# Optimization experiments

Hardware: AMD Instinct MI355X
Metric: run time of the kernel (lower is better)

The kernel has to match this reference:

```python
import jax, jax.numpy as jnp
import numpy as np

N_NODES = 349525  # complete 4-ary tree, depth 10: (4**10 - 1) / 3
X_SIZE = 128
H_SIZE = 128


def setup_inputs() -> dict:
    key = jax.random.key(0)
    ks = jax.random.split(key, 6)
    s = 0.05  # keep gates out of saturation
    return {
        "x": jax.random.normal(ks[0], (N_NODES, X_SIZE), jnp.float32),
        "W_iou": jax.random.normal(ks[1], (X_SIZE, 3 * H_SIZE), jnp.float32) * s,
        "U_iou": jax.random.normal(ks[2], (H_SIZE, 3 * H_SIZE), jnp.float32) * s,
        "b_iou": jnp.zeros((3 * H_SIZE,), jnp.float32),
        "W_f": jax.random.normal(ks[3], (X_SIZE, H_SIZE), jnp.float32) * s,
        "U_f": jax.random.normal(ks[4], (H_SIZE, H_SIZE), jnp.float32) * s,
        "b_f": jnp.zeros((H_SIZE,), jnp.float32),
        "depth": 10,
        "branching": 4,
    }


def _apply_node(iou, c_sum):
    # apply_node_func: i,o,u gates then cell/hidden update
    i, o, u = jnp.split(iou, 3, axis=-1)
    c = jax.nn.sigmoid(i) * jnp.tanh(u) + c_sum
    h = jax.nn.sigmoid(o) * jnp.tanh(c)
    return h, c


def reference(x, W_iou, U_iou, b_iou, W_f, U_f, b_f, depth, branching):
    # Nodes are in BFS order of a complete `branching`-ary forest-tree;
    # level l occupies [off[l], off[l+1]) and the children of level l are
    # exactly level l+1 (contiguous, `branching` per parent).
    H = b_f.shape[-1]
    off = [(branching ** l - 1) // (branching - 1) for l in range(depth + 1)]

    node_iou = x @ W_iou + b_iou  # [N, 3H]  (W_iou(x) + b_iou)
    node_f = x @ W_f + b_f        # [N, H]   (W_f(x) + b_f)

    h_levels = [None] * depth
    c_levels = [None] * depth

    # Leaves: mailbox empty -> h_tilda = 0, c = 0
    s, e = off[depth - 1], off[depth]
    h, c = _apply_node(node_iou[s:e], jnp.zeros((e - s, H), x.dtype))
    h_levels[depth - 1], c_levels[depth - 1] = h, c

    # Bottom-up topological propagation
    for l in range(depth - 2, -1, -1):
        s, e = off[l], off[l + 1]
        nl = e - s
        ch_h = h_levels[l + 1].reshape(nl, branching, H)  # mailbox['h']
        ch_c = c_levels[l + 1].reshape(nl, branching, H)  # mailbox['c']
        h_tilda = ch_h.sum(axis=1)
        # f = sigmoid(U_f(mailbox.h) + node_f[:, None])
        f = jax.nn.sigmoid(jnp.einsum("nkh,hg->nkg", ch_h, U_f) + node_f[s:e][:, None, :])
        c_sum = (f * ch_c).sum(axis=1)
        iou = node_iou[s:e] + h_tilda @ U_iou
        h, c = _apply_node(iou, c_sum)
        h_levels[l], c_levels[l] = h, c

    h_all = jnp.concatenate(h_levels, axis=0)
    c_all = jnp.concatenate(c_levels, axis=0)
    return h_all, c_all
```

## Files before the change

### kernel.cpp

```cpp
#include <hip/hip_runtime.h>

#define H 128

typedef __bf16 bf16x8 __attribute__((ext_vector_type(8)));
typedef float f32x4 __attribute__((ext_vector_type(4)));

__device__ __forceinline__ float fsig(float x) {
  return __builtin_amdgcn_rcpf(1.0f + __expf(-x));
}
__device__ __forceinline__ float ftanh(float x) {
  float ax = fabsf(x), e = __expf(-2.0f * ax);
  float t = (1.0f - e) * __builtin_amdgcn_rcpf(1.0f + e);
  return x < 0.0f ? -t : t;
}
__device__ __forceinline__ uint2 pack4(float a, float b, float c, float d) {
  union { __bf16 h[4]; uint2 u; } r;
  r.h[0] = (__bf16)a; r.h[1] = (__bf16)b; r.h[2] = (__bf16)c; r.h[3] = (__bf16)d;
  return r.u;
}
__device__ __forceinline__ unsigned short bfbits(float h) {
  union { __bf16 b; unsigned short u; } cv; cv.b = (__bf16)h; return cv.u;
}
__device__ __forceinline__ unsigned swz(unsigned row, unsigned colByte, unsigned rowBytes) {
  return (row * rowBytes + colByte) ^ ((row & 7) << 4);
}

__global__ __launch_bounds__(256)
void prep_weights(const float* __restrict__ W_iou, const float* __restrict__ U_iou,
                  const float* __restrict__ W_f, const float* __restrict__ U_f,
                  uint4* __restrict__ ws)
{
  int item = blockIdx.x * 256 + threadIdx.x;
  float v[8];
  if (item < 2048) {
    int fj = item >> 8, rem = item & 255, ks = rem >> 6, lane = rem & 63;
    int n = fj * 16 + (lane & 15), kb = ks * 32 + (lane >> 4) * 8;
    #pragma unroll
    for (int j = 0; j < 8; j++) v[j] = U_f[(kb + j) * H + n];
  } else if (item < 4096) {
    int i2 = item - 2048;
    int fj = i2 >> 8, rem = i2 & 255, ks = rem >> 6, lane = rem & 63;
    int n = fj * 16 + (lane & 15), kb = ks * 32 + (lane >> 4) * 8;
    #pragma unroll
    for (int j = 0; j < 8; j++) v[j] = W_f[(kb + j) * H + n];
  } else {
    int i2 = item - 4096;
    int fj = i2 >> 9, rem = i2 & 511, ks = rem >> 6, lane = rem & 63;
    int col = (fj >> 3) * 128 + (fj & 7) * 16 + (lane & 15);
    int kb = ks * 32 + (lane >> 4) * 8;
    #pragma unroll
    for (int j = 0; j < 8; j++) {
      int k = kb + j;
      v[j] = (k < 128) ? W_iou[k * 384 + col] : U_iou[(k - 128) * 384 + col];
    }
  }
  union { __bf16 h[8]; uint4 u; } r;
  #pragma unroll
  for (int j = 0; j < 8; j++) r.h[j] = (__bf16)v[j];
  ws[item] = r.u;
}

__device__ __forceinline__ void leaf_half(const char* As, const __bf16* __restrict__ iou_fmt,
                                          int j, int w, int l15, int l4, int lane,
                                          f32x4 (&acc)[4][3])
{
  #pragma unroll
  for (int ks = 0; ks < 4; ks++) {
    bf16x8 a[4], b[3];
    #pragma unroll
    for (int m = 0; m < 4; m++)
      a[m] = *reinterpret_cast<const bf16x8*>(As + swz(m * 16 + l15, (ks * 32 + l4 * 8) * 2, 256));
    #pragma unroll
    for (int g = 0; g < 3; g++) {
      int nf = g * 8 + 2 * w + j;
      b[g] = *reinterpret_cast<const bf16x8*>(iou_fmt + ((size_t)(nf * 8 + ks) * 64 + lane) * 8);
    }
    #pragma unroll
    for (int m = 0; m < 4; m++)
      #pragma unroll
      for (int g = 0; g < 3; g++)
        acc[m][g] = __builtin_amdgcn_mfma_f32_16x16x32_bf16(a[m], b[g], acc[m][g], 0, 0, 0);
  }
}

template<bool WS>
__global__ __launch_bounds__(256)
void leaf8(const float* __restrict__ x, const __bf16* __restrict__ iou_fmt,
           const float* __restrict__ b_iou,
           float* __restrict__ h_glob, float* __restrict__ c_glob,
           __bf16* __restrict__ hb_dst, int leaf_start)
{
  __shared__ __align__(16) char As[64 * 256];
  const int t = threadIdx.x;
  const int bid = blockIdx.x;
  const int m0 = leaf_start + bid * 64;
  const int lane = t & 63, w = t >> 6;
  const int l15 = lane & 15, l4 = lane >> 4;

  #pragma unroll
  for (int i = 0; i < 8; i++) {
    int idx = t + i * 256;
    int r = idx >> 5, k0 = (idx & 31) << 2;
    f32x4 v = *reinterpret_cast<const f32x4*>(&x[(size_t)(m0 + r) * H + k0]);
    *reinterpret_cast<uint2*>(As + swz(r, k0 * 2, 256)) = pack4(v.x, v.y, v.z, v.w);
  }
  __syncthreads();

  unsigned hj0p[8];

  {
    f32x4 acc[4][3] = {};
    leaf_half(As, iou_fmt, 0, w, l15, l4, lane, acc);
    int ch = 2 * w * 16 + l15;
    float bi = b_iou[ch], bo = b_iou[H + ch], bu = b_iou[2 * H + ch];
    #pragma unroll
    for (int m = 0; m < 4; m++) {
      int rowb = m * 16 + l4 * 4;
      unsigned hv[4];
      #pragma unroll
      for (int r = 0; r < 4; r++) {
        size_t o = (size_t)(m0 + rowb + r) * H + ch;
        float c = fsig(acc[m][0][r] + bi) * ftanh(acc[m][2][r] + bu);
        float h = fsig(acc[m][1][r] + bo) * ftanh(c);
        h_glob[o] = h;
        c_glob[o] = c;
        if (WS) hv[r] = bfbits(h);
      }
      if (WS) {
        hj0p[m * 2 + 0] = hv[0] | (hv[1] << 16);
        hj0p[m * 2 + 1] = hv[2] | (hv[3] << 16);
      }
    }
  }

  {
    f32x4 acc[4][3] = {};
    leaf_half(As, iou_fmt, 1, w, l15, l4, lane, acc);
    __syncthreads();
    int ch = (2 * w + 1) * 16 + l15;
    float bi = b_iou[ch], bo = b_iou[H + ch], bu = b_iou[2 * H + ch];
    #pragma unroll
    for (int m = 0; m < 4; m++) {
      int rowb = m * 16 + l4 * 4;
      #pragma unroll
      for (int r = 0; r < 4; r++) {
        size_t o = (size_t)(m0 + rowb + r) * H + ch;
        float c = fsig(acc[m][0][r] + bi) * ftanh(acc[m][2][r] + bu);
        float h = fsig(acc[m][1][r] + bo) * ftanh(c);
        h_glob[o] = h;
        c_glob[o] = c;
        if (WS)
          *reinterpret_cast<unsigned short*>(As + swz(rowb + r, ch * 2, 256)) = bfbits(h);
      }
    }
  }

  if (WS) {
    int ch0 = 2 * w * 16 + l15;
    #pragma unroll
    for (int m = 0; m < 4; m++) {
      int rowb = m * 16 + l4 * 4;
      #pragma unroll
      for (int r = 0; r < 4; r++) {
        unsigned hv = hj0p[m * 2 + (r >> 1)] >> ((r & 1) * 16);
        *reinterpret_cast<unsigned short*>(As + swz(rowb + r, ch0 * 2, 256)) = (unsigned short)hv;
      }
    }
    __syncthreads();
    char* dst = reinterpret_cast<char*>(hb_dst) + (size_t)bid * 64 * 256;
    #pragma unroll
    for (int i = 0; i < 4; i++) {
      int idx = t + i * 256;
      int row = idx >> 4, chunk = idx & 15;
      uint4 v = *reinterpret_cast<const uint4*>(As + swz(row, chunk * 16, 256));
      *reinterpret_cast<uint4*>(dst + row * 256 + chunk * 16) = v;
    }
  }
}

template<bool HB>
__device__ __forceinline__ void fused_core(
    const __bf16* __restrict__ uf_fmt, const __bf16* __restrict__ wf_fmt,
    const __bf16* __restrict__ iou_fmt,
    const float* __restrict__ b_iou, const float* __restrict__ b_f,
    float* __restrict__ h_glob, float* __restrict__ c_glob,
    int prow0, int crow0, int npar,
    char* CH, char* XH, float* SC)
{
  const int t = threadIdx.x;
  const int lane = t & 63, w = t >> 6;
  const int l15 = lane & 15, l4 = lane >> 4;

  {
    f32x4 acc[2][2] = {};
    #pragma unroll
    for (int ks = 0; ks < 4; ks++) {
      bf16x8 a[2], b[2];
      #pragma unroll
      for (int m = 0; m < 2; m++)
        a[m] = *reinterpret_cast<const bf16x8*>(XH + swz(m * 16 + l15, (ks * 32 + l4 * 8) * 2, 512));
      #pragma unroll
      for (int n = 0; n < 2; n++) {
        int nf = 2 * w + n;
        b[n] = *reinterpret_cast<const bf16x8*>(wf_fmt + ((size_t)(nf * 4 + ks) * 64 + lane) * 8);
      }
      #pragma unroll
      for (int m = 0; m < 2; m++)
        #pragma unroll
        for (int n = 0; n < 2; n++)
          acc[m][n] = __builtin_amdgcn_mfma_f32_16x16x32_bf16(a[m], b[n], acc[m][n], 0, 0, 0);
    }
    #pragma unroll
    for (int m = 0; m < 2; m++)
      #pragma unroll
      for (int n = 0; n < 2; n++)
        #pragma unroll
        for (int r = 0; r < 4; r++)
          SC[(m * 16 + l4 * 4 + r) * 128 + (2 * w + n) * 16 + l15] = acc[m][n][r];
  }
  __syncthreads();

  {
    f32x4 acc[2][8] = {};
    #pragma unroll
    for (int ks = 0; ks < 4; ks++) {
      bf16x8 a[2], b[8];
      #pragma unroll
      for (int m = 0; m < 2; m++)
        a[m] = *reinterpret_cast<const bf16x8*>(CH + swz(w * 32 + m * 16 + l15, (ks * 32 + l4 * 8) * 2, 256));
      #pragma unroll
      for (int n = 0; n < 8; n++)
        b[n] = *reinterpret_cast<const bf16x8*>(uf_fmt + ((size_t)(n * 4 + ks) * 64 + lane) * 8);
      #pragma unroll
      for (int m = 0; m < 2; m++)
        #pragma unroll
        for (int n = 0; n < 8; n++)
          acc[m][n] = __builtin_amdgcn_mfma_f32_16x16x32_bf16(a[m], b[n], acc[m][n], 0, 0, 0);
    }
    #pragma unroll
    for (int m = 0; m < 2; m++) {
      int rbase = w * 32 + m * 16 + l4 * 4;
      int ploc = rbase >> 2;
      #pragma unroll
      for (int n = 0; n < 8; n++) {
        int ch = n * 16 + l15;
        float sfx = SC[ploc * 128 + ch] + b_f[ch];
        float cs = 0.0f;
        #pragma unroll
        for (int r = 0; r < 4; r++) {
          float f = fsig(acc[m][n][r] + sfx);
          cs = fmaf(f, c_glob[(size_t)(crow0 + rbase + r) * H + ch], cs);
        }
        SC[ploc * 128 + ch] = cs;
      }
    }
  }
  __syncthreads();

  {
    f32x4 acc[2][3][2] = {};
    #pragma unroll
    for (int ks = 0; ks < 8; ks++) {
      bf16x8 a[2], b[3][2];
      #pragma unroll
      for (int m = 0; m < 2; m++)
        a[m] = *reinterpret_cast<const bf16x8*>(XH + swz(m * 16 + l15, (ks * 32 + l4 * 8) * 2, 512));
      #pragma unroll
      for (int g = 0; g < 3; g++)
        #pragma unroll
        for (int j = 0; j < 2; j++) {
          int nf = g * 8 + 2 * w + j;
          b[g][j] = *reinterpret_cast<const bf16x8*>(iou_fmt + ((size_t)(nf * 8 + ks) * 64 + lane) * 8);
        }
      #pragma unroll
      for (int m = 0; m < 2; m++)
        #pragma unroll
        for (int g = 0; g < 3; g++)
          #pragma unroll
          for (int j = 0; j < 2; j++)
            acc[m][g][j] = __builtin_amdgcn_mfma_f32_16x16x32_bf16(a[m], b[g][j], acc[m][g][j], 0, 0, 0);
    }
    #pragma unroll
    for (int j = 0; j < 2; j++) {
      int ch = (2 * w + j) * 16 + l15;
      float bi = b_iou[ch], bo = b_iou[H + ch], bu = b_iou[2 * H + ch];
      #pragma unroll
      for (int m = 0; m < 2; m++) {
        #pragma unroll
        for (int r = 0; r < 4; r++) {
          int ploc = m * 16 + l4 * 4 + r;
          if (ploc < npar) {
            float gi = acc[m][0][j][r] + bi;
            float go = acc[m][1][j][r] + bo;
            float gu = acc[m][2][j][r] + bu;
            float cs = SC[ploc * 128 + ch];
            float c = fsig(gi) * ftanh(gu) + cs;
            float h = fsig(go) * ftanh(c);
            size_t o = (size_t)(prow0 + ploc) * H + ch;
            h_glob[o] = h;
            c_glob[o] = c;
            if (HB)
              *reinterpret_cast<unsigned short*>(CH + swz(ploc, ch * 2, 256)) = bfbits(h);
          }
        }
      }
    }
  }
}

template<bool WRITE_HB>
__global__ __launch_bounds__(256)
void fused_hb(const float* __restrict__ x, const __bf16* __restrict__ uf_fmt,
              const __bf16* __restrict__ wf_fmt, const __bf16* __restrict__ iou_fmt,
              const float* __restrict__ b_iou, const float* __restrict__ b_f,
              float* __restrict__ h_glob, float* __restrict__ c_glob,
              const __bf16* __restrict__ ch_src, __bf16* __restrict__ hb_dst,
              int pstart, int cstart)
{
  __shared__ __align__(16) char CH[128 * 256];
  __shared__ __align__(16) char XH[32 * 512];
  __shared__ float SC[32 * 128];
  const int t = threadIdx.x;
  const int bid = blockIdx.x;

  {
    const char* csrc = reinterpret_cast<const char*>(ch_src) + (size_t)bid * 128 * 256;
    #pragma unroll
    for (int i = 0; i < 8; i++) {
      int idx = t + i * 256;
      int row = idx >> 4, chunk = idx & 15;
      uint4 v = *reinterpret_cast<const uint4*>(csrc + row * 256 + chunk * 16);
      *reinterpret_cast<uint4*>(CH + swz(row, chunk * 16, 256)) = v;
    }
  }
  #pragma unroll
  for (int i = 0; i < 4; i++) {
    int idx = t + i * 256;
    int p = idx >> 5, k0 = (idx & 31) << 2;
    f32x4 v = *reinterpret_cast<const f32x4*>(&x[(size_t)(pstart + bid * 32 + p) * H + k0]);
    *reinterpret_cast<uint2*>(XH + swz(p, k0 * 2, 512)) = pack4(v.x, v.y, v.z, v.w);
  }
  __syncthreads();
  #pragma unroll
  for (int i = 0; i < 2; i++) {
    int idx = t + i * 256;
    int p = idx >> 4, chunk = idx & 15;
    float s[8] = {};
    #pragma unroll
    for (int cj = 0; cj < 4; cj++) {
      union { uint4 u; __bf16 h[8]; } uv;
      uv.u = *reinterpret_cast<const uint4*>(CH + swz(4 * p + cj, chunk * 16, 256));
      #pragma unroll
      for (int e = 0; e < 8; e++) s[e] += (float)uv.h[e];
    }
    union { __bf16 h[8]; uint4 u; } ov;
    #pragma unroll
    for (int e = 0; e < 8; e++) ov.h[e] = (__bf16)s[e];
    *reinterpret_cast<uint4*>(XH + swz(p, 256 + chunk * 16, 512)) = ov.u;
  }
  __syncthreads();

  fused_core<WRITE_HB>(uf_fmt, wf_fmt, iou_fmt, b_iou, b_f, h_glob, c_glob,
                       pstart + bid * 32, cstart + bid * 128, 32, CH, XH, SC);

  if (WRITE_HB) {
    __syncthreads();
    char* dst = reinterpret_cast<char*>(hb_dst) + (size_t)bid * 32 * 256;
    #pragma unroll
    for (int i = 0; i < 2; i++) {
      int idx = t + i * 256;
      int row = idx >> 4, chunk = idx & 15;
      uint4 v = *reinterpret_cast<const uint4*>(CH + swz(row, chunk * 16, 256));
      *reinterpret_cast<uint4*>(dst + row * 256 + chunk * 16) = v;
    }
  }
}

__device__ __forceinline__ void fused_body(
    const float* __restrict__ x, const __bf16* __restrict__ uf_fmt,
    const __bf16* __restrict__ wf_fmt, const __bf16* __restrict__ iou_fmt,
    const float* __restrict__ b_iou, const float* __restrict__ b_f,
    float* __restrict__ h_glob, float* __restrict__ c_glob,
    int prow0, int crow0, int npar,
    char* CH, char* XH, float* SC)
{
  const int t = threadIdx.x;
  #pragma unroll
  for (int i = 0; i < 4; i++) {
    int idx = t + i * 256;
    int p = idx >> 5, k0 = (idx & 31) << 2;
    f32x4 s = {};
    #pragma unroll
    for (int j = 0; j < 4; j++) {
      f32x4 v = *reinterpret_cast<const f32x4*>(&h_glob[(size_t)(crow0 + p * 4 + j) * H + k0]);
      *reinterpret_cast<uint2*>(CH + swz(p * 4 + j, k0 * 2, 256)) = pack4(v.x, v.y, v.z, v.w);
      s += v;
    }
    *reinterpret_cast<uint2*>(XH + swz(p, (128 + k0) * 2, 512)) = pack4(s.x, s.y, s.z, s.w);
  }
  #pragma unroll
  for (int i = 0; i < 4; i++) {
    int idx = t + i * 256;
    int p = idx >> 5, k0 = (idx & 31) << 2;
    f32x4 v = *reinterpret_cast<const f32x4*>(&x[(size_t)(prow0 + p) * H + k0]);
    *reinterpret_cast<uint2*>(XH + swz(p, k0 * 2, 512)) = pack4(v.x, v.y, v.z, v.w);
  }
  __syncthreads();
  fused_core<false>(uf_fmt, wf_fmt, iou_fmt, b_iou, b_f, h_glob, c_glob,
                    prow0, crow0, npar, CH, XH, SC);
}

__global__ __launch_bounds__(256)
void fused_level(const float* __restrict__ x, const __bf16* __restrict__ uf_fmt,
                 const __bf16* __restrict__ wf_fmt, const __bf16* __restrict__ iou_fmt,
                 const float* __restrict__ b_iou, const float* __restrict__ b_f,
                 float* __restrict__ h_glob, float* __restrict__ c_glob,
                 int pstart, int cstart)
{
  __shared__ __align__(16) char CH[128 * 256];
  __shared__ __align__(16) char XH[32 * 512];
  __shared__ float SC[32 * 128];
  fused_body(x, uf_fmt, wf_fmt, iou_fmt, b_iou, b_f, h_glob, c_glob,
             pstart + blockIdx.x * 32, cstart + blockIdx.x * 128, 32, CH, XH, SC);
}

#define SNR 4
#define SRP 2
#define BR 4

__global__ __launch_bounds__(256)
void small_kernel(const float* __restrict__ x,
                  const float* __restrict__ W_iou, const float* __restrict__ b_iou,
                  const float* __restrict__ U_iou, const float* __restrict__ W_f,
                  const float* __restrict__ U_f, const float* __restrict__ b_f,
                  float* __restrict__ h_out, float* __restrict__ c_out,
                  int lvl_start, int child_start, int n_lvl)
{
  __shared__ float xs[SNR][H];
  __shared__ float hs[SNR * BR][H];
  __shared__ float ht[SNR][H];
  const int t = threadIdx.x;
  const int node0 = blockIdx.x * SNR;
  const int nrows = min(SNR, n_lvl - node0);

  {
    const f32x4* xgv = reinterpret_cast<const f32x4*>(x + (size_t)(lvl_start + node0) * H);
    f32x4* xsv = reinterpret_cast<f32x4*>(&xs[0][0]);
    int total = nrows * (H / 4);
    for (int i = t; i < total; i += 256) xsv[i] = xgv[i];
  }
  {
    const f32x4* hgv = reinterpret_cast<const f32x4*>(h_out + (size_t)(child_start + node0 * BR) * H);
    f32x4* hsv = reinterpret_cast<f32x4*>(&hs[0][0]);
    int total = nrows * BR * (H / 4);
    for (int i = t; i < total; i += 256) hsv[i] = hgv[i];
  }
  __syncthreads();

  const int ch = t & (H - 1);
  const int g = t >> 7;

  float fx[SRP], ai[SRP], ao[SRP], au[SRP];
  {
    float bi = b_iou[ch], bo = b_iou[ch + H], bu = b_iou[ch + 2 * H], bf = b_f[ch];
    #pragma unroll
    for (int r = 0; r < SRP; r++) { fx[r] = bf; ai[r] = bi; ao[r] = bo; au[r] = bu; }
  }
  {
    const float* wfp = W_f + ch;
    const float* wip = W_iou + ch;
    #pragma unroll 4
    for (int k = 0; k < H; k++) {
      float wf = wfp[k * H];
      float w0 = wip[k * 384], w1 = wip[k * 384 + H], w2 = wip[k * 384 + 2 * H];
      #pragma unroll
      for (int r = 0; r < SRP; r++) {
        float xk = xs[g * SRP + r][k];
        fx[r] = fmaf(xk, wf, fx[r]);
        ai[r] = fmaf(xk, w0, ai[r]);
        ao[r] = fmaf(xk, w1, ao[r]);
        au[r] = fmaf(xk, w2, au[r]);
      }
    }
  }
  #pragma unroll
  for (int r = 0; r < SRP; r++) {
    int row = g * SRP + r;
    float s = hs[row * BR + 0][ch] + hs[row * BR + 1][ch]
            + hs[row * BR + 2][ch] + hs[row * BR + 3][ch];
    ht[row][ch] = s;
  }
  __syncthreads();

  float z[BR][SRP];
  #pragma unroll
  for (int kc = 0; kc < BR; kc++)
    #pragma unroll
    for (int r = 0; r < SRP; r++) z[kc][r] = fx[r];
  {
    const float* ufp = U_f + ch;
    #pragma unroll 4
    for (int m = 0; m < H; m++) {
      float uf = ufp[m * H];
      #pragma unroll
      for (int kc = 0; kc < BR; kc++)
        #pragma unroll
        for (int r = 0; r < SRP; r++)
          z[kc][r] = fmaf(hs[(g * SRP + r) * BR + kc][m], uf, z[kc][r]);
    }
  }
  float csum[SRP];
  #pragma unroll
  for (int r = 0; r < SRP; r++) csum[r] = 0.0f;
  #pragma unroll
  for (int kc = 0; kc < BR; kc++) {
    #pragma unroll
    for (int r = 0; r < SRP; r++) {
      size_t childnode = (size_t)child_start + (size_t)(node0 + g * SRP + r) * BR + kc;
      float f = fsig(z[kc][r]);
      csum[r] = fmaf(f, c_out[childnode * H + ch], csum[r]);
    }
  }
  {
    const float* uip = U_iou + ch;
    #pragma unroll 4
    for (int m = 0; m < H; m++) {
      float w0 = uip[m * 384], w1 = uip[m * 384 + H], w2 = uip[m * 384 + 2 * H];
      #pragma unroll
      for (int r = 0; r < SRP; r++) {
        float hm = ht[g * SRP + r][m];
        ai[r] = fmaf(hm, w0, ai[r]);
        ao[r] = fmaf(hm, w1, ao[r]);
        au[r] = fmaf(hm, w2, au[r]);
      }
    }
  }
  #pragma unroll
  for (int r = 0; r < SRP; r++) {
    int row = g * SRP + r;
    if (row < nrows) {
      float c = fsig(ai[r]) * ftanh(au[r]) + csum[r];
      float h = fsig(ao[r]) * ftanh(c);
      size_t node = (size_t)(lvl_start + node0 + row);
      h_out[node * H + ch] = h;
      c_out[node * H + ch] = c;
    }
  }
}

extern "C" void kernel_launch(void* const* d_in, const int* in_sizes, int n_in,
                              void* d_out, int out_size, void* d_ws, size_t ws_size,
                              hipStream_t stream)
{
  const float* x     = (const float*)d_in[0];
  const float* W_iou = (const float*)d_in[1];
  const float* U_iou = (const float*)d_in[2];
  const float* b_iou = (const float*)d_in[3];
  const float* W_f   = (const float*)d_in[4];
  const float* U_f   = (const float*)d_in[5];
  const float* b_f   = (const float*)d_in[6];
  const int N = 349525;

  float* h_out = (float*)d_out;
  float* c_out = h_out + (size_t)N * H;

  const __bf16* uf_fmt  = (const __bf16*)d_ws;
  const __bf16* wf_fmt  = (const __bf16*)d_ws + 16384;
  const __bf16* iou_fmt = (const __bf16*)d_ws + 32768;
  __bf16* hb16 = (__bf16*)((char*)d_ws + 262144);
  __bf16* hb_l8 = hb16 + (size_t)262144 * 128;

  const bool use_ws = ws_size >= (262144ULL + 83886080ULL);

  int off[11];
  off[0] = 0;
  for (int l = 1; l <= 10; l++) off[l] = off[l - 1] * 4 + 1;

  prep_weights<<<64, 256, 0, stream>>>(W_iou, U_iou, W_f, U_f, (uint4*)d_ws);

  if (use_ws) {
    leaf8<true><<<4096, 256, 0, stream>>>(x, iou_fmt, b_iou, h_out, c_out, hb16, off[9]);
    fused_hb<true><<<2048, 256, 0, stream>>>(x, uf_fmt, wf_fmt, iou_fmt, b_iou, b_f,
                                             h_out, c_out, hb16, hb_l8, off[8], off[9]);
    fused_hb<false><<<512, 256, 0, stream>>>(x, uf_fmt, wf_fmt, iou_fmt, b_iou, b_f,
                                             h_out, c_out, hb_l8, nullptr, off[7], off[8]);
  } else {
    leaf8<false><<<4096, 256, 0, stream>>>(x, iou_fmt, b_iou, h_out, c_out, nullptr, off[9]);
    fused_level<<<2048, 256, 0, stream>>>(x, uf_fmt, wf_fmt, iou_fmt, b_iou, b_f,
                                          h_out, c_out, off[8], off[9]);
    fused_level<<<512, 256, 0, stream>>>(x, uf_fmt, wf_fmt, iou_fmt, b_iou, b_f,
                                         h_out, c_out, off[7], off[8]);
  }

  for (int l = 6; l >= 4; l--) {
    int n_par = off[l + 1] - off[l];
    fused_level<<<n_par / 32, 256, 0, stream>>>(x, uf_fmt, wf_fmt, iou_fmt, b_iou, b_f,
                                                h_out, c_out, off[l], off[l + 1]);
  }

  for (int l = 3; l >= 0; l--) {
    int s = off[l], e = off[l + 1];
    int n = e - s;
    int grid = (n + SNR - 1) / SNR;
    small_kernel<<<grid, 256, 0, stream>>>(x, W_iou, b_iou, U_iou, W_f, U_f, b_f,
                                           h_out, c_out, s, e, n);
  }
}
```

Before: 384.9 us.

## Split fused level kernels across 512 threads with one MFMA column tile per wave

Fused internal-level kernels now launch 512 threads (8 waves) instead of 256, and each wave handles half the previous MFMA tiles. The W_f and iou GEMMs give each wave one 16-column tile instead of two, and the U_f child GEMM gives each wave 16 child rows instead of 32. Load and store loops are rescaled to match. This aims to raise wave-level parallelism and cut per-thread register pressure for latency hiding, at the cost of more waves per block and more redundant A-fragment loads from LDS.

```diff
diff --git a/kernel.cpp b/kernel.cpp
--- a/kernel.cpp
+++ b/kernel.cpp
@@ -179,7 +179,7 @@
 }
 
 template<bool HB>
-__device__ __forceinline__ void fused_core(
+__device__ __forceinline__ void fused_core512(
     const __bf16* __restrict__ uf_fmt, const __bf16* __restrict__ wf_fmt,
     const __bf16* __restrict__ iou_fmt,
     const float* __restrict__ b_iou, const float* __restrict__ b_f,
@@ -192,116 +192,94 @@
   const int l15 = lane & 15, l4 = lane >> 4;
 
   {
-    f32x4 acc[2][2] = {};
+    f32x4 acc[2] = {};
     #pragma unroll
     for (int ks = 0; ks < 4; ks++) {
-      bf16x8 a[2], b[2];
+      bf16x8 a[2], b;
       #pragma unroll
       for (int m = 0; m < 2; m++)
         a[m] = *reinterpret_cast<const bf16x8*>(XH + swz(m * 16 + l15, (ks * 32 + l4 * 8) * 2, 512));
-      #pragma unroll
-      for (int n = 0; n < 2; n++) {
-        int nf = 2 * w + n;
-        b[n] = *reinterpret_cast<const bf16x8*>(wf_fmt + ((size_t)(nf * 4 + ks) * 64 + lane) * 8);
-      }
+      b = *reinterpret_cast<const bf16x8*>(wf_fmt + ((size_t)(w * 4 + ks) * 64 + lane) * 8);
       #pragma unroll
       for (int m = 0; m < 2; m++)
-        #pragma unroll
-        for (int n = 0; n < 2; n++)
-          acc[m][n] = __builtin_amdgcn_mfma_f32_16x16x32_bf16(a[m], b[n], acc[m][n], 0, 0, 0);
+        acc[m] = __builtin_amdgcn_mfma_f32_16x16x32_bf16(a[m], b, acc[m], 0, 0, 0);
     }
     #pragma unroll
     for (int m = 0; m < 2; m++)
       #pragma unroll
-      for (int n = 0; n < 2; n++)
-        #pragma unroll
-        for (int r = 0; r < 4; r++)
-          SC[(m * 16 + l4 * 4 + r) * 128 + (2 * w + n) * 16 + l15] = acc[m][n][r];
-  }
-  __syncthreads();
-
-  {
-    f32x4 acc[2][8] = {};
+      for (int r = 0; r < 4; r++)
+        SC[(m * 16 + l4 * 4 + r) * 128 + w * 16 + l15] = acc[m][r];
+  }
+  __syncthreads();
+
+  {
+    f32x4 acc[8] = {};
     #pragma unroll
     for (int ks = 0; ks < 4; ks++) {
-      bf16x8 a[2], b[8];
-      #pragma unroll
-      for (int m = 0; m < 2; m++)
-        a[m] = *reinterpret_cast<const bf16x8*>(CH + swz(w * 32 + m * 16 + l15, (ks * 32 + l4 * 8) * 2, 256));
+      bf16x8 a, b[8];
+      a = *reinterpret_cast<const bf16x8*>(CH + swz(w * 16 + l15, (ks * 32 + l4 * 8) * 2, 256));
       #pragma unroll
       for (int n = 0; n < 8; n++)
         b[n] = *reinterpret_cast<const bf16x8*>(uf_fmt + ((size_t)(n * 4 + ks) * 64 + lane) * 8);
       #pragma unroll
-      for (int m = 0; m < 2; m++)
-        #pragma unroll
-        for (int n = 0; n < 8; n++)
-          acc[m][n] = __builtin_amdgcn_mfma_f32_16x16x32_bf16(a[m], b[n], acc[m][n], 0, 0, 0);
-    }
-    #pragma unroll
-    for (int m = 0; m < 2; m++) {
-      int rbase = w * 32 + m * 16 + l4 * 4;
-      int ploc = rbase >> 2;
-      #pragma unroll
-      for (int n = 0; n < 8; n++) {
-        int ch = n * 16 + l15;
-        float sfx = SC[ploc * 128 + ch] + b_f[ch];
-        float cs = 0.0f;
-        #pragma unroll
-        for (int r = 0; r < 4; r++) {
-          float f = fsig(acc[m][n][r] + sfx);
-          cs = fmaf(f, c_glob[(size_t)(crow0 + rbase + r) * H + ch], cs);
-        }
-        SC[ploc * 128 + ch] = cs;
-      }
-    }
-  }
-  __syncthreads();
-
-  {
-    f32x4 acc[2][3][2] = {};
+      for (int n = 0; n < 8; n++)
+        acc[n] = __builtin_amdgcn_mfma_f32_16x16x32_bf16(a, b[n], acc[n], 0, 0, 0);
+    }
+    int rbase = w * 16 + l4 * 4;
+    int ploc = rbase >> 2;
+    #pragma unroll
+    for (int n = 0; n < 8; n++) {
+      int ch = n * 16 + l15;
+      float sfx = SC[ploc * 128 + ch] + b_f[ch];
+      float cs = 0.0f;
+      #pragma unroll
+      for (int r = 0; r < 4; r++) {
+        float f = fsig(acc[n][r] + sfx);
+        cs = fmaf(f, c_glob[(size_t)(crow0 + rbase + r) * H + ch], cs);
+      }
+      SC[ploc * 128 + ch] = cs;
+    }
+  }
+  __syncthreads();
+
+  {
+    f32x4 acc[2][3] = {};
     #pragma unroll
     for (int ks = 0; ks < 8; ks++) {
-      bf16x8 a[2], b[3][2];
+      bf16x8 a[2], b[3];
       #pragma unroll
       for (int m = 0; m < 2; m++)
         a[m] = *reinterpret_cast<const bf16x8*>(XH + swz(m * 16 + l15, (ks * 32 + l4 * 8) * 2, 512));
       #pragma unroll
-      for (int g = 0; g < 3; g++)
-        #pragma unroll
-        for (int j = 0; j < 2; j++) {
-          int nf = g * 8 + 2 * w + j;
-          b[g][j] = *reinterpret_cast<const bf16x8*>(iou_fmt + ((size_t)(nf * 8 + ks) * 64 + lane) * 8);
-        }
+      for (int g = 0; g < 3; g++) {
+        int nf = g * 8 + w;
+        b[g] = *reinterpret_cast<const bf16x8*>(iou_fmt + ((size_t)(nf * 8 + ks) * 64 + lane) * 8);
+      }
       #pragma unroll
       for (int m = 0; m < 2; m++)
         #pragma unroll
         for (int g = 0; g < 3; g++)
-          #pragma unroll
-          for (int j = 0; j < 2; j++)
-            acc[m][g][j] = __builtin_amdgcn_mfma_f32_16x16x32_bf16(a[m], b[g][j], acc[m][g][j], 0, 0, 0);
-    }
-    #pragma unroll
-    for (int j = 0; j < 2; j++) {
-      int ch = (2 * w + j) * 16 + l15;
-      float bi = b_iou[ch], bo = b_iou[H + ch], bu = b_iou[2 * H + ch];
-      #pragma unroll
-      for (int m = 0; m < 2; m++) {
-        #pragma unroll
-        for (int r = 0; r < 4; r++) {
-          int ploc = m * 16 + l4 * 4 + r;
-          if (ploc < npar) {
-            float gi = acc[m][0][j][r] + bi;
-            float go = acc[m][1][j][r] + bo;
-            float gu = acc[m][2][j][r] + bu;
-            float cs = SC[ploc * 128 + ch];
-            float c = fsig(gi) * ftanh(gu) + cs;
-            float h = fsig(go) * ftanh(c);
-            size_t o = (size_t)(prow0 + ploc) * H + ch;
-            h_glob[o] = h;
-            c_glob[o] = c;
-            if (HB)
-              *reinterpret_cast<unsigned short*>(CH + swz(ploc, ch * 2, 256)) = bfbits(h);
-          }
+          acc[m][g] = __builtin_amdgcn_mfma_f32_16x16x32_bf16(a[m], b[g], acc[m][g], 0, 0, 0);
+    }
+    int ch = w * 16 + l15;
+    float bi = b_iou[ch], bo = b_iou[H + ch], bu = b_iou[2 * H + ch];
+    #pragma unroll
+    for (int m = 0; m < 2; m++) {
+      #pragma unroll
+      for (int r = 0; r < 4; r++) {
+        int ploc = m * 16 + l4 * 4 + r;
+        if (ploc < npar) {
+          float gi = acc[m][0][r] + bi;
+          float go = acc[m][1][r] + bo;
+          float gu = acc[m][2][r] + bu;
+          float cs = SC[ploc * 128 + ch];
+          float c = fsig(gi) * ftanh(gu) + cs;
+          float h = fsig(go) * ftanh(c);
+          size_t o = (size_t)(prow0 + ploc) * H + ch;
+          h_glob[o] = h;
+          c_glob[o] = c;
+          if (HB)
+            *reinterpret_cast<unsigned short*>(CH + swz(ploc, ch * 2, 256)) = bfbits(h);
         }
       }
     }
@@ -309,7 +287,7 @@
 }
 
 template<bool WRITE_HB>
-__global__ __launch_bounds__(256)
+__global__ __launch_bounds__(512)
 void fused_hb(const float* __restrict__ x, const __bf16* __restrict__ uf_fmt,
               const __bf16* __restrict__ wf_fmt, const __bf16* __restrict__ iou_fmt,
               const float* __restrict__ b_iou, const float* __restrict__ b_f,
@@ -326,25 +304,23 @@
   {
     const char* csrc = reinterpret_cast<const char*>(ch_src) + (size_t)bid * 128 * 256;
     #pragma unroll
-    for (int i = 0; i < 8; i++) {
-      int idx = t + i * 256;
+    for (int i = 0; i < 4; i++) {
+      int idx = t + i * 512;
       int row = idx >> 4, chunk = idx & 15;
       uint4 v = *reinterpret_cast<const uint4*>(csrc + row * 256 + chunk * 16);
       *reinterpret_cast<uint4*>(CH + swz(row, chunk * 16, 256)) = v;
     }
   }
   #pragma unroll
-  for (int i = 0; i < 4; i++) {
-    int idx = t + i * 256;
+  for (int i = 0; i < 2; i++) {
+    int idx = t + i * 512;
     int p = idx >> 5, k0 = (idx & 31) << 2;
     f32x4 v = *reinterpret_cast<const f32x4*>(&x[(size_t)(pstart + bid * 32 + p) * H + k0]);
     *reinterpret_cast<uint2*>(XH + swz(p, k0 * 2, 512)) = pack4(v.x, v.y, v.z, v.w);
   }
   __syncthreads();
-  #pragma unroll
-  for (int i = 0; i < 2; i++) {
-    int idx = t + i * 256;
-    int p = idx >> 4, chunk = idx & 15;
+  {
+    int p = t >> 4, chunk = t & 15;
     float s[8] = {};
     #pragma unroll
     for (int cj = 0; cj < 4; cj++) {
@@ -360,57 +336,19 @@
   }
   __syncthreads();
 
-  fused_core<WRITE_HB>(uf_fmt, wf_fmt, iou_fmt, b_iou, b_f, h_glob, c_glob,
-                       pstart + bid * 32, cstart + bid * 128, 32, CH, XH, SC);
+  fused_core512<WRITE_HB>(uf_fmt, wf_fmt, iou_fmt, b_iou, b_f, h_glob, c_glob,
+                          pstart + bid * 32, cstart + bid * 128, 32, CH, XH, SC);
 
   if (WRITE_HB) {
     __syncthreads();
     char* dst = reinterpret_cast<char*>(hb_dst) + (size_t)bid * 32 * 256;
-    #pragma unroll
-    for (int i = 0; i < 2; i++) {
-      int idx = t + i * 256;
-      int row = idx >> 4, chunk = idx & 15;
-      uint4 v = *reinterpret_cast<const uint4*>(CH + swz(row, chunk * 16, 256));
-      *reinterpret_cast<uint4*>(dst + row * 256 + chunk * 16) = v;
-    }
-  }
-}
-
-__device__ __forceinline__ void fused_body(
-    const float* __restrict__ x, const __bf16* __restrict__ uf_fmt,
-    const __bf16* __restrict__ wf_fmt, const __bf16* __restrict__ iou_fmt,
-    const float* __restrict__ b_iou, const float* __restrict__ b_f,
-    float* __restrict__ h_glob, float* __restrict__ c_glob,
-    int prow0, int crow0, int npar,
-    char* CH, char* XH, float* SC)
-{
-  const int t = threadIdx.x;
-  #pragma unroll
-  for (int i = 0; i < 4; i++) {
-    int idx = t + i * 256;
-    int p = idx >> 5, k0 = (idx & 31) << 2;
-    f32x4 s = {};
-    #pragma unroll
-    for (int j = 0; j < 4; j++) {
-      f32x4 v = *reinterpret_cast<const f32x4*>(&h_glob[(size_t)(crow0 + p * 4 + j) * H + k0]);
-      *reinterpret_cast<uint2*>(CH + swz(p * 4 + j, k0 * 2, 256)) = pack4(v.x, v.y, v.z, v.w);
-      s += v;
-    }
-    *reinterpret_cast<uint2*>(XH + swz(p, (128 + k0) * 2, 512)) = pack4(s.x, s.y, s.z, s.w);
-  }
-  #pragma unroll
-  for (int i = 0; i < 4; i++) {
-    int idx = t + i * 256;
-    int p = idx >> 5, k0 = (idx & 31) << 2;
-    f32x4 v = *reinterpret_cast<const f32x4*>(&x[(size_t)(prow0 + p) * H + k0]);
-    *reinterpret_cast<uint2*>(XH + swz(p, k0 * 2, 512)) = pack4(v.x, v.y, v.z, v.w);
-  }
-  __syncthreads();
-  fused_core<false>(uf_fmt, wf_fmt, iou_fmt, b_iou, b_f, h_glob, c_glob,
-                    prow0, crow0, npar, CH, XH, SC);
-}
-
-__global__ __launch_bounds__(256)
+    int row = t >> 4, chunk = t & 15;
+    uint4 v = *reinterpret_cast<const uint4*>(CH + swz(row, chunk * 16, 256));
+    *reinterpret_cast<uint4*>(dst + row * 256 + chunk * 16) = v;
+  }
+}
+
+__global__ __launch_bounds__(512)
 void fused_level(const float* __restrict__ x, const __bf16* __restrict__ uf_fmt,
                  const __bf16* __restrict__ wf_fmt, const __bf16* __restrict__ iou_fmt,
                  const float* __restrict__ b_iou, const float* __restrict__ b_f,
@@ -420,8 +358,33 @@
   __shared__ __align__(16) char CH[128 * 256];
   __shared__ __align__(16) char XH[32 * 512];
   __shared__ float SC[32 * 128];
-  fused_body(x, uf_fmt, wf_fmt, iou_fmt, b_iou, b_f, h_glob, c_glob,
-             pstart + blockIdx.x * 32, cstart + blockIdx.x * 128, 32, CH, XH, SC);
+  const int t = threadIdx.x;
+  const int prow0 = pstart + blockIdx.x * 32;
+  const int crow0 = cstart + blockIdx.x * 128;
+
+  #pragma unroll
+  for (int i = 0; i < 2; i++) {
+    int idx = t + i * 512;
+    int p = idx >> 5, k0 = (idx & 31) << 2;
+    f32x4 s = {};
+    #pragma unroll
+    for (int j = 0; j < 4; j++) {
+      f32x4 v = *reinterpret_cast<const f32x4*>(&h_glob[(size_t)(crow0 + p * 4 + j) * H + k0]);
+      *reinterpret_cast<uint2*>(CH + swz(p * 4 + j, k0 * 2, 256)) = pack4(v.x, v.y, v.z, v.w);
+      s += v;
+    }
+    *reinterpret_cast<uint2*>(XH + swz(p, (128 + k0) * 2, 512)) = pack4(s.x, s.y, s.z, s.w);
+  }
+  #pragma unroll
+  for (int i = 0; i < 2; i++) {
+    int idx = t + i * 512;
+    int p = idx >> 5, k0 = (idx & 31) << 2;
+    f32x4 v = *reinterpret_cast<const f32x4*>(&x[(size_t)(prow0 + p) * H + k0]);
+    *reinterpret_cast<uint2*>(XH + swz(p, k0 * 2, 512)) = pack4(v.x, v.y, v.z, v.w);
+  }
+  __syncthreads();
+  fused_core512<false>(uf_fmt, wf_fmt, iou_fmt, b_iou, b_f, h_glob, c_glob,
+                       prow0, crow0, 32, CH, XH, SC);
 }
 
 #define SNR 4
@@ -580,21 +543,21 @@
 
   if (use_ws) {
     leaf8<true><<<4096, 256, 0, stream>>>(x, iou_fmt, b_iou, h_out, c_out, hb16, off[9]);
-    fused_hb<true><<<2048, 256, 0, stream>>>(x, uf_fmt, wf_fmt, iou_fmt, b_iou, b_f,
+    fused_hb<true><<<2048, 512, 0, stream>>>(x, uf_fmt, wf_fmt, iou_fmt, b_iou, b_f,
                                              h_out, c_out, hb16, hb_l8, off[8], off[9]);
-    fused_hb<false><<<512, 256, 0, stream>>>(x, uf_fmt, wf_fmt, iou_fmt, b_iou, b_f,
+    fused_hb<false><<<512, 512, 0, stream>>>(x, uf_fmt, wf_fmt, iou_fmt, b_iou, b_f,
                                              h_out, c_out, hb_l8, nullptr, off[7], off[8]);
   } else {
     leaf8<false><<<4096, 256, 0, stream>>>(x, iou_fmt, b_iou, h_out, c_out, nullptr, off[9]);
-    fused_level<<<2048, 256, 0, stream>>>(x, uf_fmt, wf_fmt, iou_fmt, b_iou, b_f,
+    fused_level<<<2048, 512, 0, stream>>>(x, uf_fmt, wf_fmt, iou_fmt, b_iou, b_f,
                                           h_out, c_out, off[8], off[9]);
-    fused_level<<<512, 256, 0, stream>>>(x, uf_fmt, wf_fmt, iou_fmt, b_iou, b_f,
+    fused_level<<<512, 512, 0, stream>>>(x, uf_fmt, wf_fmt, iou_fmt, b_iou, b_f,
                                          h_out, c_out, off[7], off[8]);
   }
 
   for (int l = 6; l >= 4; l--) {
     int n_par = off[l + 1] - off[l];
-    fused_level<<<n_par / 32, 256, 0, stream>>>(x, uf_fmt, wf_fmt, iou_fmt, b_iou, b_f,
+    fused_level<<<n_par / 32, 512, 0, stream>>>(x, uf_fmt, wf_fmt, iou_fmt, b_iou, b_f,
                                                 h_out, c_out, off[l], off[l + 1]);
   }
 
```

After: 385.8 us. Within noise of the previous version (+0.2%).
